# Performance work log

Hardware: AMD Instinct MI355X
Metric: run time of the kernel (lower is better)

## Reference

```python
import jax, jax.numpy as jnp
import numpy as np


def setup_inputs() -> dict:
    key = jax.random.key(0)
    ks = jax.random.split(key, 6)
    B, S, E, H = 8, 2048, 1024, 64
    scale = 1.0 / np.sqrt(E)
    return {
        "query": jax.random.normal(ks[0], (B, S, E), dtype=jnp.float32),
        "key": jax.random.normal(ks[1], (B, S, E), dtype=jnp.float32),
        "value": jax.random.normal(ks[2], (B, S, E), dtype=jnp.float32),
        "Wq": jax.random.normal(ks[3], (E, H), dtype=jnp.float32) * scale,
        "bq": jnp.zeros((H,), dtype=jnp.float32),
        "Wk": jax.random.normal(ks[4], (E, H), dtype=jnp.float32) * scale,
        "bk": jnp.zeros((H,), dtype=jnp.float32),
        "Wv": jax.random.normal(ks[5], (E, H), dtype=jnp.float32) * scale,
        "bv": jnp.zeros((H,), dtype=jnp.float32),
    }


def reference(query, key, value, Wq, bq, Wk, bk, Wv, bv):
    # Linear projections: [B,S,E] @ [E,H] + [H] -> [B,S,H]
    q = jnp.einsum("bse,eh->bsh", query, Wq) + bq
    k = jnp.einsum("bse,eh->bsh", key, Wk) + bk
    v = jnp.einsum("bse,eh->bsh", value, Wv) + bv
    head_dim = q.shape[-1]
    # scores [B,S,S], softmax over last axis, then weighted sum of values
    scores = jnp.einsum("bqh,bkh->bqk", q, k) / jnp.sqrt(
        jnp.asarray(head_dim, dtype=q.dtype)
    )
    attn = jax.nn.softmax(scores, axis=-1)
    return jnp.einsum("bqk,bkh->bqh", attn, v)
```

## Files before the change

kernel.cpp:

```cpp
#include <hip/hip_runtime.h>
#include <math.h>

#define BB 8
#define SS 2048
#define EE 1024
#define HH 64
#define MM (BB * SS)

typedef unsigned short u16;
typedef __attribute__((ext_vector_type(8))) short short8;
typedef __attribute__((ext_vector_type(4))) float floatx4;

__device__ __forceinline__ u16 f2bf(float f) {
    union { float f; unsigned u; } a; a.f = f;
    unsigned r = a.u + 0x7fffu + ((a.u >> 16) & 1u);
    return (u16)(r >> 16);
}

__device__ __forceinline__ void split2(float f0, float f1, unsigned& hp, unsigned& lp) {
    union { float f; unsigned u; } a0, a1, h0, h1, l0, l1;
    a0.f = f0; a1.f = f1;
    h0.u = a0.u & 0xffff0000u;
    h1.u = a1.u & 0xffff0000u;
    l0.f = f0 - h0.f;
    l1.f = f1 - h1.f;
    hp = __builtin_amdgcn_perm(a1.u, a0.u, 0x07060302u);
    lp = __builtin_amdgcn_perm(l1.u, l0.u, 0x07060302u);
}

#define WP_MAT 131072

__global__ __launch_bounds__(512) void pack_w(
    const float* __restrict__ W0, const float* __restrict__ W1, const float* __restrict__ W2,
    u16* __restrict__ Wp)
{
    const int which = blockIdx.y;
    const float* __restrict__ W = (which == 0) ? W0 : (which == 1) ? W1 : W2;
    const int t    = blockIdx.x;
    const int tid  = threadIdx.x;
    const int ks   = tid >> 8;
    const int nt   = (tid >> 6) & 3;
    const int lane = tid & 63;
    const int n    = lane & 15;
    const int g    = lane >> 4;

    const int k0 = t * 64 + ks * 32 + g * 8;
    const int c  = nt * 16 + n;

    float e[8];
    #pragma unroll
    for (int j = 0; j < 8; ++j) e[j] = W[(size_t)(k0 + j) * HH + c];

    unsigned hp[4], lp[4];
    #pragma unroll
    for (int i = 0; i < 4; ++i) split2(e[2 * i], e[2 * i + 1], hp[i], lp[i]);

    u16* dst = Wp + (size_t)which * WP_MAT
                  + ((size_t)(t * 8 + ks * 4 + nt) * 2) * 512 + lane * 8;
    *(uint4*)dst         = (uint4){hp[0], hp[1], hp[2], hp[3]};
    *(uint4*)(dst + 512) = (uint4){lp[0], lp[1], lp[2], lp[3]};
}

#define BMROWS 64
#define NCHUNK (EE / 64)

__global__ __launch_bounds__(256) void proj_mfma(
    const float* __restrict__ A0, const float* __restrict__ A1, const float* __restrict__ A2,
    const u16* __restrict__ Wp,
    const float* __restrict__ b0, const float* __restrict__ b1, const float* __restrict__ b2,
    u16* __restrict__ o0, u16* __restrict__ o1, u16* __restrict__ o2)
{
    const int which = blockIdx.y;
    const float* __restrict__ A    = (which == 0) ? A0 : (which == 1) ? A1 : A2;
    const float* __restrict__ bias = (which == 0) ? b0 : (which == 1) ? b1 : b2;
    u16* __restrict__ out          = (which == 0) ? o0 : (which == 1) ? o1 : o2;

    const int tid  = threadIdx.x;
    const int lane = tid & 63;
    const int wave = tid >> 6;
    const int n    = lane & 15;
    const int g    = lane >> 4;
    const int row0 = blockIdx.x * BMROWS;

    const float* __restrict__ ap = A + (size_t)(row0 + wave * 16 + n) * EE + g * 8;
    const u16* __restrict__ wpb = Wp + (size_t)which * WP_MAT + lane * 8;

    floatx4 acc[4];
    #pragma unroll
    for (int nt = 0; nt < 4; ++nt) acc[nt] = (floatx4){0.f, 0.f, 0.f, 0.f};

    float4 av[4];
    av[0] = *(const float4*)(ap + 0);
    av[1] = *(const float4*)(ap + 4);
    av[2] = *(const float4*)(ap + 32);
    av[3] = *(const float4*)(ap + 36);

    for (int t = 0; t < NCHUNK; ++t) {
        float4 ac[4];
        #pragma unroll
        for (int i = 0; i < 4; ++i) ac[i] = av[i];

        if (t + 1 < NCHUNK) {
            const float* apn = ap + (t + 1) * 64;
            av[0] = *(const float4*)(apn + 0);
            av[1] = *(const float4*)(apn + 4);
            av[2] = *(const float4*)(apn + 32);
            av[3] = *(const float4*)(apn + 36);
        }

        const u16* wpc = wpb + (size_t)t * 8192;

        #pragma unroll
        for (int ks = 0; ks < 2; ++ks) {
            unsigned hp0, lp0, hp1, lp1, hp2, lp2, hp3, lp3;
            split2(ac[ks * 2].x,     ac[ks * 2].y,     hp0, lp0);
            split2(ac[ks * 2].z,     ac[ks * 2].w,     hp1, lp1);
            split2(ac[ks * 2 + 1].x, ac[ks * 2 + 1].y, hp2, lp2);
            split2(ac[ks * 2 + 1].z, ac[ks * 2 + 1].w, hp3, lp3);
            union { uint4 u; short8 s; } ch, cl;
            ch.u = (uint4){hp0, hp1, hp2, hp3};
            cl.u = (uint4){lp0, lp1, lp2, lp3};
            const short8 ah = ch.s, al = cl.s;

            #pragma unroll
            for (int nt = 0; nt < 4; ++nt) {
                const short8 whf = *(const short8*)(wpc + ((ks * 4 + nt) * 2 + 0) * 512);
                const short8 wlf = *(const short8*)(wpc + ((ks * 4 + nt) * 2 + 1) * 512);
                acc[nt] = __builtin_amdgcn_mfma_f32_16x16x32_bf16(ah, whf, acc[nt], 0, 0, 0);
                acc[nt] = __builtin_amdgcn_mfma_f32_16x16x32_bf16(al, whf, acc[nt], 0, 0, 0);
                acc[nt] = __builtin_amdgcn_mfma_f32_16x16x32_bf16(ah, wlf, acc[nt], 0, 0, 0);
            }
        }
    }

    #pragma unroll
    for (int nt = 0; nt < 4; ++nt) {
        const float bv = bias[nt * 16 + n];
        #pragma unroll
        for (int r = 0; r < 4; ++r) {
            const int row = row0 + wave * 16 + g * 4 + r;
            out[(size_t)row * HH + nt * 16 + n] = f2bf(acc[nt][r] + bv);
        }
    }
}

__global__ __launch_bounds__(256) void flash_mfma(
    const u16* __restrict__ qp, const u16* __restrict__ kp,
    const u16* __restrict__ vp, float* __restrict__ out)
{
    __shared__ __align__(16) u16 Ks[2][64 * 64];
    __shared__ __align__(16) u16 Vt[2][64 * 64];
    __shared__ __align__(16) u16 Pw[4][16 * 72];

    const int b    = blockIdx.y;
    const int q0   = blockIdx.x * 32;
    const int tid  = threadIdx.x;
    const int lane = tid & 63;
    const int wave = tid >> 6;
    const int wq   = wave & 1;
    const int ks   = wave >> 1;
    const int n    = lane & 15;
    const int g    = lane >> 4;

    const u16* qrow = qp + ((size_t)b * SS + q0 + wq * 16 + n) * HH;
    const short8 qa0 = *(const short8*)(qrow + g * 8);
    const short8 qa1 = *(const short8*)(qrow + 32 + g * 8);

    floatx4 Oa[4];
    #pragma unroll
    for (int ht = 0; ht < 4; ++ht) Oa[ht] = (floatx4){0.f, 0.f, 0.f, 0.f};
    float m_i[4], l_i[4];
    #pragma unroll
    for (int r = 0; r < 4; ++r) { m_i[r] = -1e30f; l_i[r] = 0.f; }

    const u16* kb = kp + (size_t)b * SS * HH;
    const u16* vb = vp + (size_t)b * SS * HH;

    const int jK0 = tid >> 3, jK1 = 32 + (tid >> 3), cs = tid & 7;
    const int jV  = (tid & 15) * 4, hV = (tid >> 4) * 4;

    short8  kr0, kr1;
    ushort4 vr0, vr1, vr2, vr3;

    kr0 = *(const short8*)(kb + (size_t)jK0 * HH + cs * 8);
    kr1 = *(const short8*)(kb + (size_t)jK1 * HH + cs * 8);
    vr0 = *(const ushort4*)(vb + (size_t)(jV + 0) * HH + hV);
    vr1 = *(const ushort4*)(vb + (size_t)(jV + 1) * HH + hV);
    vr2 = *(const ushort4*)(vb + (size_t)(jV + 2) * HH + hV);
    vr3 = *(const ushort4*)(vb + (size_t)(jV + 3) * HH + hV);
    {
        *(short8*)&Ks[0][jK0 * 64 + ((cs ^ (jK0 & 7)) << 3)] = kr0;
        *(short8*)&Ks[0][jK1 * 64 + ((cs ^ (jK1 & 7)) << 3)] = kr1;
        const u16* a0 = (const u16*)&vr0; const u16* a1 = (const u16*)&vr1;
        const u16* a2 = (const u16*)&vr2; const u16* a3 = (const u16*)&vr3;
        #pragma unroll
        for (int i = 0; i < 4; ++i) {
            const int h = hV + i;
            ushort4 w; w.x = a0[i]; w.y = a1[i]; w.z = a2[i]; w.w = a3[i];
            *(ushort4*)((char*)&Vt[0][0] + h * 128 + (((jV >> 3) ^ (h & 7)) << 4) + ((jV & 4) << 1)) = w;
        }
    }
    __syncthreads();

    for (int t = 0; t < SS / 64; ++t) {
        const int cur = t & 1;

        if (t + 1 < SS / 64) {
            const size_t kt = (size_t)(t + 1) * 64;
            kr0 = *(const short8*)(kb + (kt + jK0) * HH + cs * 8);
            kr1 = *(const short8*)(kb + (kt + jK1) * HH + cs * 8);
            vr0 = *(const ushort4*)(vb + (kt + jV + 0) * HH + hV);
            vr1 = *(const ushort4*)(vb + (kt + jV + 1) * HH + hV);
            vr2 = *(const ushort4*)(vb + (kt + jV + 2) * HH + hV);
            vr3 = *(const ushort4*)(vb + (kt + jV + 3) * HH + hV);
        }

        floatx4 S[2];
        #pragma unroll
        for (int nt = 0; nt < 2; ++nt) {
            const int j = ks * 32 + nt * 16 + n;
            const short8 kf0 = *(const short8*)&Ks[cur][j * 64 + (((0 + g) ^ (j & 7)) << 3)];
            const short8 kf1 = *(const short8*)&Ks[cur][j * 64 + (((4 + g) ^ (j & 7)) << 3)];
            floatx4 a = (floatx4){0.f, 0.f, 0.f, 0.f};
            a = __builtin_amdgcn_mfma_f32_16x16x32_bf16(qa0, kf0, a, 0, 0, 0);
            a = __builtin_amdgcn_mfma_f32_16x16x32_bf16(qa1, kf1, a, 0, 0, 0);
            S[nt] = a;
        }

        float mx[4];
        #pragma unroll
        for (int r = 0; r < 4; ++r) mx[r] = -1e30f;
        #pragma unroll
        for (int nt = 0; nt < 2; ++nt)
            #pragma unroll
            for (int r = 0; r < 4; ++r) {
                S[nt][r] *= 0.125f;
                mx[r] = fmaxf(mx[r], S[nt][r]);
            }
        #pragma unroll
        for (int off = 8; off >= 1; off >>= 1)
            #pragma unroll
            for (int r = 0; r < 4; ++r)
                mx[r] = fmaxf(mx[r], __shfl_xor(mx[r], off, 64));

        float alpha[4], ps[4];
        #pragma unroll
        for (int r = 0; r < 4; ++r) {
            const float Mn = fmaxf(m_i[r], mx[r]);
            alpha[r] = __expf(m_i[r] - Mn);
            m_i[r]   = Mn;
            ps[r]    = 0.f;
        }
        float p[2][4];
        #pragma unroll
        for (int nt = 0; nt < 2; ++nt)
            #pragma unroll
            for (int r = 0; r < 4; ++r) {
                p[nt][r] = __expf(S[nt][r] - m_i[r]);
                ps[r] += p[nt][r];
            }
        #pragma unroll
        for (int off = 8; off >= 1; off >>= 1)
            #pragma unroll
            for (int r = 0; r < 4; ++r)
                ps[r] += __shfl_xor(ps[r], off, 64);
        #pragma unroll
        for (int r = 0; r < 4; ++r) l_i[r] = l_i[r] * alpha[r] + ps[r];
        #pragma unroll
        for (int ht = 0; ht < 4; ++ht)
            #pragma unroll
            for (int r = 0; r < 4; ++r) Oa[ht][r] *= alpha[r];

        #pragma unroll
        for (int nt = 0; nt < 2; ++nt)
            #pragma unroll
            for (int r = 0; r < 4; ++r)
                Pw[wave][(g * 4 + r) * 72 + nt * 16 + n] = f2bf(p[nt][r]);
        const short8 pa = *(const short8*)&Pw[wave][n * 72 + g * 8];

        #pragma unroll
        for (int ht = 0; ht < 4; ++ht) {
            const int h = ht * 16 + n;
            const short8 vf = *(const short8*)((const char*)&Vt[cur][0] + h * 128 +
                                               ((((ks << 2) + g) ^ (h & 7)) << 4));
            Oa[ht] = __builtin_amdgcn_mfma_f32_16x16x32_bf16(pa, vf, Oa[ht], 0, 0, 0);
        }

        if (t + 1 < SS / 64) {
            const int nx = cur ^ 1;
            *(short8*)&Ks[nx][jK0 * 64 + ((cs ^ (jK0 & 7)) << 3)] = kr0;
            *(short8*)&Ks[nx][jK1 * 64 + ((cs ^ (jK1 & 7)) << 3)] = kr1;
            const u16* a0 = (const u16*)&vr0; const u16* a1 = (const u16*)&vr1;
            const u16* a2 = (const u16*)&vr2; const u16* a3 = (const u16*)&vr3;
            #pragma unroll
            for (int i = 0; i < 4; ++i) {
                const int h = hV + i;
                ushort4 w; w.x = a0[i]; w.y = a1[i]; w.z = a2[i]; w.w = a3[i];
                *(ushort4*)((char*)&Vt[nx][0] + h * 128 + (((jV >> 3) ^ (h & 7)) << 4) + ((jV & 4) << 1)) = w;
            }
        }
        __syncthreads();
    }

    float* Cb = (float*)&Ks[0][0];
    float* Cm = Cb + 2 * 16 * 68;
    float* Cl = Cm + 32;
    if (ks == 1) {
        #pragma unroll
        for (int ht = 0; ht < 4; ++ht)
            #pragma unroll
            for (int r = 0; r < 4; ++r)
                Cb[(wq * 16 + g * 4 + r) * 68 + ht * 16 + n] = Oa[ht][r];
        if (n == 0)
            #pragma unroll
            for (int r = 0; r < 4; ++r) {
                Cm[wq * 16 + g * 4 + r] = m_i[r];
                Cl[wq * 16 + g * 4 + r] = l_i[r];
            }
    }
    __syncthreads();
    if (ks == 0) {
        float a0v[4], a1v[4], linv[4];
        #pragma unroll
        for (int r = 0; r < 4; ++r) {
            const int m = g * 4 + r;
            const float m1 = Cm[wq * 16 + m], l1 = Cl[wq * 16 + m];
            const float M  = fmaxf(m_i[r], m1);
            const float e0 = __expf(m_i[r] - M), e1 = __expf(m1 - M);
            a0v[r] = e0; a1v[r] = e1;
            linv[r] = 1.f / (l_i[r] * e0 + l1 * e1);
        }
        #pragma unroll
        for (int ht = 0; ht < 4; ++ht)
            #pragma unroll
            for (int r = 0; r < 4; ++r) {
                const float o1 = Cb[(wq * 16 + g * 4 + r) * 68 + ht * 16 + n];
                const float v  = (Oa[ht][r] * a0v[r] + o1 * a1v[r]) * linv[r];
                out[((size_t)b * SS + q0 + wq * 16 + g * 4 + r) * HH + ht * 16 + n] = v;
            }
    }
}

extern "C" void kernel_launch(void* const* d_in, const int* in_sizes, int n_in,
                              void* d_out, int out_size, void* d_ws, size_t ws_size,
                              hipStream_t stream) {
    const float* query = (const float*)d_in[0];
    const float* key   = (const float*)d_in[1];
    const float* value = (const float*)d_in[2];
    const float* Wq    = (const float*)d_in[3];
    const float* bq    = (const float*)d_in[4];
    const float* Wk    = (const float*)d_in[5];
    const float* bk    = (const float*)d_in[6];
    const float* Wv    = (const float*)d_in[7];
    const float* bv    = (const float*)d_in[8];
    float* out = (float*)d_out;

    u16* qp = (u16*)d_ws;
    u16* kp = qp + (size_t)MM * HH;
    u16* vp = kp + (size_t)MM * HH;
    u16* Wp = vp + (size_t)MM * HH;

    dim3 wgrid(NCHUNK, 3);
    pack_w<<<wgrid, 512, 0, stream>>>(Wq, Wk, Wv, Wp);

    dim3 pgrid(MM / BMROWS, 3);
    proj_mfma<<<pgrid, 256, 0, stream>>>(query, key, value,
                                         Wp,
                                         bq, bk, bv,
                                         qp, kp, vp);

    dim3 agrid(SS / 32, BB);
    flash_mfma<<<agrid, 256, 0, stream>>>(qp, kp, vp, out);
}
```

Measured before the change: 290.5 us.

## Split projection K across wave pairs and fold softmax scale into Wq

The projection kernel now gives each block 32 rows and splits the 1024-wide reduction between two waves per row group. The two partial sums are combined through shared memory, which doubles the grid and should improve memory-level parallelism. The A-operand prefetch is deepened to two chunks, and launch bounds request 6 blocks per SM. The 1/sqrt(H) score scale is folded into Wq and bq during packing, removing a multiply in the flash loop at the cost of a small rounding difference in the projected q.

```diff
diff --git a/kernel.cpp b/kernel.cpp
--- a/kernel.cpp
+++ b/kernel.cpp
@@ -36,6 +36,7 @@
 {
     const int which = blockIdx.y;
     const float* __restrict__ W = (which == 0) ? W0 : (which == 1) ? W1 : W2;
+    const float scale = (which == 0) ? 0.125f : 1.0f;
     const int t    = blockIdx.x;
     const int tid  = threadIdx.x;
     const int ks   = tid >> 8;
@@ -49,7 +50,7 @@
 
     float e[8];
     #pragma unroll
-    for (int j = 0; j < 8; ++j) e[j] = W[(size_t)(k0 + j) * HH + c];
+    for (int j = 0; j < 8; ++j) e[j] = W[(size_t)(k0 + j) * HH + c] * scale;
 
     unsigned hp[4], lp[4];
     #pragma unroll
@@ -61,10 +62,9 @@
     *(uint4*)(dst + 512) = (uint4){lp[0], lp[1], lp[2], lp[3]};
 }
 
-#define BMROWS 64
-#define NCHUNK (EE / 64)
-
-__global__ __launch_bounds__(256) void proj_mfma(
+#define PCH 8
+
+__global__ __launch_bounds__(256, 6) void proj_mfma(
     const float* __restrict__ A0, const float* __restrict__ A1, const float* __restrict__ A2,
     const u16* __restrict__ Wp,
     const float* __restrict__ b0, const float* __restrict__ b1, const float* __restrict__ b2,
@@ -74,72 +74,92 @@
     const float* __restrict__ A    = (which == 0) ? A0 : (which == 1) ? A1 : A2;
     const float* __restrict__ bias = (which == 0) ? b0 : (which == 1) ? b1 : b2;
     u16* __restrict__ out          = (which == 0) ? o0 : (which == 1) ? o1 : o2;
+    const float bscale = (which == 0) ? 0.125f : 1.0f;
+
+    __shared__ float Cb[2][16][68];
 
     const int tid  = threadIdx.x;
     const int lane = tid & 63;
     const int wave = tid >> 6;
+    const int kh   = wave & 1;
+    const int rg   = wave >> 1;
     const int n    = lane & 15;
     const int g    = lane >> 4;
-    const int row0 = blockIdx.x * BMROWS;
-
-    const float* __restrict__ ap = A + (size_t)(row0 + wave * 16 + n) * EE + g * 8;
-    const u16* __restrict__ wpb = Wp + (size_t)which * WP_MAT + lane * 8;
+    const int row0 = blockIdx.x * 32 + rg * 16;
+
+    const float* __restrict__ ap = A + (size_t)(row0 + n) * EE + kh * (PCH * 64) + g * 8;
+    const u16* __restrict__ wpb = Wp + (size_t)which * WP_MAT + (size_t)kh * PCH * 8192 + lane * 8;
 
     floatx4 acc[4];
     #pragma unroll
     for (int nt = 0; nt < 4; ++nt) acc[nt] = (floatx4){0.f, 0.f, 0.f, 0.f};
 
-    float4 av[4];
-    av[0] = *(const float4*)(ap + 0);
-    av[1] = *(const float4*)(ap + 4);
-    av[2] = *(const float4*)(ap + 32);
-    av[3] = *(const float4*)(ap + 36);
-
-    for (int t = 0; t < NCHUNK; ++t) {
-        float4 ac[4];
-        #pragma unroll
-        for (int i = 0; i < 4; ++i) ac[i] = av[i];
-
-        if (t + 1 < NCHUNK) {
-            const float* apn = ap + (t + 1) * 64;
-            av[0] = *(const float4*)(apn + 0);
-            av[1] = *(const float4*)(apn + 4);
-            av[2] = *(const float4*)(apn + 32);
-            av[3] = *(const float4*)(apn + 36);
-        }
-
-        const u16* wpc = wpb + (size_t)t * 8192;
-
+    float4 av[2][4];
+    #pragma unroll
+    for (int s = 0; s < 2; ++s) {
+        const float* p = ap + s * 64;
+        av[s][0] = *(const float4*)(p + 0);
+        av[s][1] = *(const float4*)(p + 4);
+        av[s][2] = *(const float4*)(p + 32);
+        av[s][3] = *(const float4*)(p + 36);
+    }
+
+    for (int t = 0; t < PCH; ++t) {
+        const int cur = t & 1;
+
+        short8 ah[2], al[2];
         #pragma unroll
         for (int ks = 0; ks < 2; ++ks) {
             unsigned hp0, lp0, hp1, lp1, hp2, lp2, hp3, lp3;
-            split2(ac[ks * 2].x,     ac[ks * 2].y,     hp0, lp0);
-            split2(ac[ks * 2].z,     ac[ks * 2].w,     hp1, lp1);
-            split2(ac[ks * 2 + 1].x, ac[ks * 2 + 1].y, hp2, lp2);
-            split2(ac[ks * 2 + 1].z, ac[ks * 2 + 1].w, hp3, lp3);
+            split2(av[cur][ks * 2].x,     av[cur][ks * 2].y,     hp0, lp0);
+            split2(av[cur][ks * 2].z,     av[cur][ks * 2].w,     hp1, lp1);
+            split2(av[cur][ks * 2 + 1].x, av[cur][ks * 2 + 1].y, hp2, lp2);
+            split2(av[cur][ks * 2 + 1].z, av[cur][ks * 2 + 1].w, hp3, lp3);
             union { uint4 u; short8 s; } ch, cl;
             ch.u = (uint4){hp0, hp1, hp2, hp3};
             cl.u = (uint4){lp0, lp1, lp2, lp3};
-            const short8 ah = ch.s, al = cl.s;
-
+            ah[ks] = ch.s; al[ks] = cl.s;
+        }
+
+        if (t + 2 < PCH) {
+            const float* p = ap + (t + 2) * 64;
+            av[cur][0] = *(const float4*)(p + 0);
+            av[cur][1] = *(const float4*)(p + 4);
+            av[cur][2] = *(const float4*)(p + 32);
+            av[cur][3] = *(const float4*)(p + 36);
+        }
+
+        const u16* wpc = wpb + t * 8192;
+        #pragma unroll
+        for (int ks = 0; ks < 2; ++ks)
             #pragma unroll
             for (int nt = 0; nt < 4; ++nt) {
                 const short8 whf = *(const short8*)(wpc + ((ks * 4 + nt) * 2 + 0) * 512);
                 const short8 wlf = *(const short8*)(wpc + ((ks * 4 + nt) * 2 + 1) * 512);
-                acc[nt] = __builtin_amdgcn_mfma_f32_16x16x32_bf16(ah, whf, acc[nt], 0, 0, 0);
-                acc[nt] = __builtin_amdgcn_mfma_f32_16x16x32_bf16(al, whf, acc[nt], 0, 0, 0);
-                acc[nt] = __builtin_amdgcn_mfma_f32_16x16x32_bf16(ah, wlf, acc[nt], 0, 0, 0);
-            }
-        }
-    }
-
-    #pragma unroll
-    for (int nt = 0; nt < 4; ++nt) {
-        const float bv = bias[nt * 16 + n];
-        #pragma unroll
-        for (int r = 0; r < 4; ++r) {
-            const int row = row0 + wave * 16 + g * 4 + r;
-            out[(size_t)row * HH + nt * 16 + n] = f2bf(acc[nt][r] + bv);
+                acc[nt] = __builtin_amdgcn_mfma_f32_16x16x32_bf16(ah[ks], whf, acc[nt], 0, 0, 0);
+                acc[nt] = __builtin_amdgcn_mfma_f32_16x16x32_bf16(al[ks], whf, acc[nt], 0, 0, 0);
+                acc[nt] = __builtin_amdgcn_mfma_f32_16x16x32_bf16(ah[ks], wlf, acc[nt], 0, 0, 0);
+            }
+    }
+
+    if (kh == 1) {
+        #pragma unroll
+        for (int nt = 0; nt < 4; ++nt)
+            #pragma unroll
+            for (int r = 0; r < 4; ++r)
+                Cb[rg][g * 4 + r][nt * 16 + n] = acc[nt][r];
+    }
+    __syncthreads();
+    if (kh == 0) {
+        #pragma unroll
+        for (int nt = 0; nt < 4; ++nt) {
+            const float bv = bias[nt * 16 + n] * bscale;
+            #pragma unroll
+            for (int r = 0; r < 4; ++r) {
+                const int row = row0 + g * 4 + r;
+                const float v = acc[nt][r] + Cb[rg][g * 4 + r][nt * 16 + n] + bv;
+                out[(size_t)row * HH + nt * 16 + n] = f2bf(v);
+            }
         }
     }
 }
@@ -233,10 +253,8 @@
         #pragma unroll
         for (int nt = 0; nt < 2; ++nt)
             #pragma unroll
-            for (int r = 0; r < 4; ++r) {
-                S[nt][r] *= 0.125f;
+            for (int r = 0; r < 4; ++r)
                 mx[r] = fmaxf(mx[r], S[nt][r]);
-            }
         #pragma unroll
         for (int off = 8; off >= 1; off >>= 1)
             #pragma unroll
@@ -360,10 +378,10 @@
     u16* vp = kp + (size_t)MM * HH;
     u16* Wp = vp + (size_t)MM * HH;
 
-    dim3 wgrid(NCHUNK, 3);
+    dim3 wgrid(EE / 64, 3);
     pack_w<<<wgrid, 512, 0, stream>>>(Wq, Wk, Wv, Wp);
 
-    dim3 pgrid(MM / BMROWS, 3);
+    dim3 pgrid(MM / 32, 3);
     proj_mfma<<<pgrid, 256, 0, stream>>>(query, key, value,
                                          Wp,
                                          bq, bk, bv,
```

Result: no change. 291.2 us (+0.2%).
